# Kernel optimization log

Hardware: AMD Instinct MI355X
Metric: run time of the kernel (lower is better)

Reference implementation:

```python
import jax, jax.numpy as jnp
import numpy as np

CHUNK = 128
EPS = 1e-6


def setup_inputs() -> dict:
    key = jax.random.key(0)
    k1, k2, k3 = jax.random.split(key, 3)
    B, H, N, D, E = 4, 8, 4096, 64, 64
    q = jax.random.uniform(k1, (B, H, N, D), dtype=jnp.float32)
    k = jax.random.uniform(k2, (B, H, N, D), dtype=jnp.float32)
    v = jax.random.normal(k3, (B, H, N, E), dtype=jnp.float32)
    return {"q": q, "k": k, "v": v, "inferrring_states": 1}


def reference(q, k, v, inferrring_states):
    # infer_hidden_states path: chunked causal linear attention with carried state.
    B, H, N, D = q.shape
    E = v.shape[-1]
    nc = N // CHUNK
    # [nc, B, H, CHUNK, *] for scan over chunks
    qc = jnp.moveaxis(q.reshape(B, H, nc, CHUNK, D), 2, 0)
    kc = jnp.moveaxis(k.reshape(B, H, nc, CHUNK, D), 2, 0)
    vc = jnp.moveaxis(v.reshape(B, H, nc, CHUNK, E), 2, 0)

    Z0 = jnp.zeros((B, H, 1, D), dtype=q.dtype)        # running sum of k
    S0 = jnp.zeros((B, H, 1, D, E), dtype=q.dtype)     # running sum of k v^T

    def step(carry, qkv):
        Z, S = carry
        qi, ki, vi = qkv
        k_cumsum = Z + jnp.cumsum(ki, axis=-2)                      # [B,H,C,D]
        D_inv = 1.0 / jnp.einsum('bhnd,bhnd->bhn', qi, k_cumsum + EPS)
        context = jnp.einsum('bhnd,bhne->bhnde', ki, vi)            # [B,H,C,D,E]
        ctx_cumsum = S + jnp.cumsum(context, axis=-3)
        out = jnp.einsum('bhnde,bhnd,bhn->bhne', ctx_cumsum, qi, D_inv)
        new_carry = (k_cumsum[:, :, -1:], ctx_cumsum[:, :, -1:])
        return new_carry, out

    (Z, S), outs = jax.lax.scan(step, (Z0, S0), (qc, kc, vc))
    out = jnp.moveaxis(outs, 0, 2).reshape(B, H, N, E)
    # states: Z=[B,H,D], S=[B,H,D,E]
    return out, Z[:, :, 0], S[:, :, 0]
```

## Files before the change

### kernel.cpp

```cpp
#include <hip/hip_runtime.h>


#define CHUNKSZ 128
#define DD 64
#define EE 64
#define NC 32
#define NBH 32
#define NSEQ 4096
#define EPSV 1e-6f
#define OUT0 (NBH * NSEQ * EE)
#define KV_ELEMS (NBH * NC * DD * EE)

typedef short bf16x8 __attribute__((ext_vector_type(8)));
typedef short bf16x4 __attribute__((ext_vector_type(4)));
typedef float f32x4  __attribute__((ext_vector_type(4)));

__device__ __forceinline__ unsigned short f2bf(float f) {
    union { float f; unsigned u; } x; x.f = f;
    unsigned u = x.u + 0x7FFFu + ((x.u >> 16) & 1u);
    return (unsigned short)(u >> 16);
}
__device__ __forceinline__ float bf2f(unsigned short s) {
    union { unsigned u; float f; } x; x.u = ((unsigned)s) << 16;
    return x.f;
}

__global__ __launch_bounds__(256) void la_phase1(
    const float* __restrict__ k, const float* __restrict__ v,
    float* __restrict__ kv, float* __restrict__ ks)
{
    const int blk = blockIdx.x;
    const int bh = blk / NC, c = blk % NC;
    const size_t rowbase = (size_t)bh * NSEQ + (size_t)c * CHUNKSZ;

    __shared__ alignas(16) unsigned short kT[CHUNKSZ * DD];
    __shared__ alignas(16) unsigned short vT[CHUNKSZ * EE];
    __shared__ float ksp[4][DD];

    char* kb = (char*)kT;
    char* vb = (char*)vT;

    const int t = threadIdx.x;
    const int w = t >> 6, l = t & 63;
    const int lg = l >> 4, lm = l & 15;

    float kpart[4] = {0.f, 0.f, 0.f, 0.f};
    {
        const float4* kg = (const float4*)(k + rowbase * DD);
        const float4* vg = (const float4*)(v + rowbase * EE);
        const int d0 = (t & 15) * 4;
#pragma unroll
        for (int i = 0; i < 8; ++i) {
            int idx = t + 256 * i;
            int m = idx >> 4;
            float4 f = kg[idx];
            kpart[0] += f.x; kpart[1] += f.y; kpart[2] += f.z; kpart[3] += f.w;
            int base = (m >> 3) * 1024 + (m & 7) * 2;
            *(unsigned short*)(kb + base + (d0 + 0) * 16) = f2bf(f.x);
            *(unsigned short*)(kb + base + (d0 + 1) * 16) = f2bf(f.y);
            *(unsigned short*)(kb + base + (d0 + 2) * 16) = f2bf(f.z);
            *(unsigned short*)(kb + base + (d0 + 3) * 16) = f2bf(f.w);
        }
#pragma unroll
        for (int i = 0; i < 8; ++i) {
            int idx = t + 256 * i;
            int m = idx >> 4;
            float4 f = vg[idx];
            int base = (m >> 3) * 1024 + (m & 7) * 2;
            *(unsigned short*)(vb + base + (d0 + 0) * 16) = f2bf(f.x);
            *(unsigned short*)(vb + base + (d0 + 1) * 16) = f2bf(f.y);
            *(unsigned short*)(vb + base + (d0 + 2) * 16) = f2bf(f.z);
            *(unsigned short*)(vb + base + (d0 + 3) * 16) = f2bf(f.w);
        }
    }
#pragma unroll
    for (int j = 0; j < 4; ++j) {
        kpart[j] += __shfl_xor(kpart[j], 16);
        kpart[j] += __shfl_xor(kpart[j], 32);
    }
    if (l < 16) {
#pragma unroll
        for (int j = 0; j < 4; ++j) ksp[w][l * 4 + j] = kpart[j];
    }
    __syncthreads();

    f32x4 acc[4] = {};
#pragma unroll
    for (int kk = 0; kk < 4; ++kk) {
        bf16x8 aK = *(bf16x8*)(kb + (lg + 4 * kk) * 1024 + (16 * w + lm) * 16);
#pragma unroll
        for (int ei = 0; ei < 4; ++ei) {
            bf16x8 bV = *(bf16x8*)(vb + (lg + 4 * kk) * 1024 + (16 * ei + lm) * 16);
            acc[ei] = __builtin_amdgcn_mfma_f32_16x16x32_bf16(aK, bV, acc[ei], 0, 0, 0);
        }
    }
    float* kvout = kv + (size_t)(bh * NC + c) * DD * EE;
#pragma unroll
    for (int ei = 0; ei < 4; ++ei) {
#pragma unroll
        for (int r = 0; r < 4; ++r) {
            int d = 16 * w + 4 * lg + r;
            kvout[(size_t)d * EE + 16 * ei + lm] = acc[ei][r];
        }
    }
    if (t < DD)
        ks[(size_t)(bh * NC + c) * DD + t] = ksp[0][t] + ksp[1][t] + ksp[2][t] + ksp[3][t];
}

__global__ __launch_bounds__(64) void la_phase2(
    float* __restrict__ kv, float* __restrict__ ks, float* __restrict__ out)
{
    const int bid = blockIdx.x, t = threadIdx.x;
    if (bid < 512) {
        const int gid = bid * 64 + t;
        const int bh = gid >> 10;
        const int rem = gid & 1023;
        float* base = kv + (size_t)bh * (NC * DD * EE) + (size_t)rem * 4;
        float4 vals[32];
#pragma unroll
        for (int c = 0; c < 32; ++c)
            vals[c] = *(const float4*)(base + (size_t)c * (DD * EE));
        float4 run = {0.f, 0.f, 0.f, 0.f};
#pragma unroll
        for (int c = 0; c < 32; ++c) {
            float4 x = vals[c];
            *(float4*)(base + (size_t)c * (DD * EE)) = run;
            run.x += x.x; run.y += x.y; run.z += x.z; run.w += x.w;
        }
        *(float4*)(out + OUT0 + NBH * DD + (size_t)gid * 4) = run;
    } else {
        const int tid = (bid - 512) * 64 + t;
        const int bh = tid >> 6, d = tid & 63;
        float vals[32];
#pragma unroll
        for (int c = 0; c < 32; ++c)
            vals[c] = ks[(size_t)(bh * NC + c) * DD + d];
        float run = 0.f;
#pragma unroll
        for (int c = 0; c < 32; ++c) {
            float x = vals[c];
            ks[(size_t)(bh * NC + c) * DD + d] = run;
            run += x;
        }
        out[OUT0 + tid] = run;
    }
}

__global__ __launch_bounds__(256) void la_phase3(
    const float* __restrict__ q, const float* __restrict__ k,
    const float* __restrict__ v, const float* __restrict__ kv,
    const float* __restrict__ ks, float* __restrict__ out)
{
    const int blk = blockIdx.x;
    const int bh = blk / NC, c = blk % NC;
    const size_t rowbase = (size_t)bh * NSEQ + (size_t)c * CHUNKSZ;

    __shared__ alignas(16) unsigned short k_lds[CHUNKSZ * DD];
    __shared__ alignas(16) unsigned short v_lds[CHUNKSZ * EE];
    __shared__ alignas(16) unsigned short s_lds[CHUNKSZ * CHUNKSZ];
    __shared__ alignas(16) unsigned short st_lds[DD * EE];
    __shared__ float dinv_lds[CHUNKSZ];

    char* kb  = (char*)k_lds;
    char* vb  = (char*)v_lds;
    char* sb  = (char*)s_lds;
    char* stb = (char*)st_lds;

    const int t  = threadIdx.x;
    const int w  = t >> 6;
    const int l  = t & 63;
    const int lg = l >> 4;
    const int lm = l & 15;

    {
        bf16x8 z = {0,0,0,0,0,0,0,0};
#pragma unroll
        for (int i = 0; i < 8; ++i)
            *(bf16x8*)(sb + t * 128 + i * 16) = z;
    }
    {
        const float4* kg = (const float4*)(k + rowbase * DD);
#pragma unroll
        for (int i = 0; i < 8; ++i) {
            int idx = t + i * 256;
            int m = idx >> 4, c4 = idx & 15;
            float4 f = kg[idx];
            bf16x4 u;
            u[0] = (short)f2bf(f.x); u[1] = (short)f2bf(f.y);
            u[2] = (short)f2bf(f.z); u[3] = (short)f2bf(f.w);
            int byt = m * 128 + ((c4 * 8) ^ ((m & 7) << 4));
            *(bf16x4*)(kb + byt) = u;
        }
    }
    {
        const float4* vg = (const float4*)(v + rowbase * EE);
#pragma unroll
        for (int i = 0; i < 8; ++i) {
            int idx = t + i * 256;
            int m = idx >> 4, e0 = (idx & 15) * 4;
            float4 f = vg[idx];
            int base = (m >> 3) * 1024 + (m & 7) * 2;
            *(unsigned short*)(vb + base + (e0 + 0) * 16) = f2bf(f.x);
            *(unsigned short*)(vb + base + (e0 + 1) * 16) = f2bf(f.y);
            *(unsigned short*)(vb + base + (e0 + 2) * 16) = f2bf(f.z);
            *(unsigned short*)(vb + base + (e0 + 3) * 16) = f2bf(f.w);
        }
    }
    {
        const float4* sg = (const float4*)(kv + ((size_t)(bh * NC + c) * DD) * EE);
#pragma unroll
        for (int i = 0; i < 4; ++i) {
            int idx = t + i * 256;
            int d = idx >> 4, e0 = (idx & 15) * 4;
            float4 f = sg[idx];
            float ff[4] = {f.x, f.y, f.z, f.w};
#pragma unroll
            for (int j = 0; j < 4; ++j) {
                int e = e0 + j;
                int byt = e * 128 + ((d * 2) ^ ((e & 7) << 4));
                *(unsigned short*)(stb + byt) = f2bf(ff[j]);
            }
        }
    }
    bf16x8 a_q[2][2];
#pragma unroll
    for (int ni2 = 0; ni2 < 2; ++ni2) {
        int ni = w + 4 * ni2;
        const float* qrow = q + (rowbase + 16 * ni + lm) * DD;
#pragma unroll
        for (int kk = 0; kk < 2; ++kk) {
            const float4* p = (const float4*)(qrow + 8 * lg + 32 * kk);
            float4 f0 = p[0], f1 = p[1];
            bf16x8 u;
            u[0] = (short)f2bf(f0.x); u[1] = (short)f2bf(f0.y);
            u[2] = (short)f2bf(f0.z); u[3] = (short)f2bf(f0.w);
            u[4] = (short)f2bf(f1.x); u[5] = (short)f2bf(f1.y);
            u[6] = (short)f2bf(f1.z); u[7] = (short)f2bf(f1.w);
            a_q[ni2][kk] = u;
        }
    }
    __syncthreads();

#pragma unroll
    for (int ni2 = 0; ni2 < 2; ++ni2) {
        const int ni = w + 4 * ni2;
        for (int mi = 0; mi <= ni; ++mi) {
            f32x4 cc = {0.f, 0.f, 0.f, 0.f};
            const int m = 16 * mi + lm;
#pragma unroll
            for (int kk = 0; kk < 2; ++kk) {
                int byt = m * 128 + (((8 * lg + 32 * kk) * 2) ^ ((m & 7) << 4));
                bf16x8 bk = *(bf16x8*)(kb + byt);
                cc = __builtin_amdgcn_mfma_f32_16x16x32_bf16(a_q[ni2][kk], bk, cc, 0, 0, 0);
            }
            const int nbase = 16 * ni + 4 * lg;
#pragma unroll
            for (int r = 0; r < 4; ++r) {
                int n = nbase + r;
                float val = (m <= n) ? cc[r] : 0.f;
                int byt = n * 256 + ((m * 2) ^ ((n & 7) << 4));
                *(unsigned short*)(sb + byt) = f2bf(val);
            }
        }
    }
    __syncthreads();

    {
        const int n = t >> 1, h = t & 1;
        float ssum = 0.f;
#pragma unroll
        for (int s8 = 0; s8 < 8; ++s8) {
            int byt = n * 256 + ((128 * h + 16 * s8) ^ ((n & 7) << 4));
            bf16x8 sv = *(bf16x8*)(sb + byt);
#pragma unroll
            for (int j = 0; j < 8; ++j) ssum += bf2f((unsigned short)sv[j]);
        }
        const float* qrow = q + (rowbase + n) * DD + 32 * h;
        const float* Zi = ks + (size_t)(bh * NC + c) * DD + 32 * h;
        float qdot = 0.f, qs = 0.f;
#pragma unroll
        for (int d = 0; d < 32; ++d) {
            float qf = qrow[d];
            qdot += qf * Zi[d];
            qs += qf;
        }
        float tot = ssum + qdot + EPSV * qs;
        tot += __shfl_xor(tot, 1);
        if (h == 0) dinv_lds[n] = 1.f / tot;
    }

    f32x4 acc[2][4];
#pragma unroll
    for (int ni2 = 0; ni2 < 2; ++ni2) {
        const int ni = w + 4 * ni2;
        const int kmax = (ni >> 1) + 1;
#pragma unroll
        for (int ei = 0; ei < 4; ++ei) {
            f32x4 cc = {0.f, 0.f, 0.f, 0.f};
            const int e = 16 * ei + lm;
#pragma unroll
            for (int kk = 0; kk < 2; ++kk) {
                int byt = e * 128 + (((8 * lg + 32 * kk) * 2) ^ ((e & 7) << 4));
                bf16x8 bs = *(bf16x8*)(stb + byt);
                cc = __builtin_amdgcn_mfma_f32_16x16x32_bf16(a_q[ni2][kk], bs, cc, 0, 0, 0);
            }
            const int n = 16 * ni + lm;
            for (int kk = 0; kk < kmax; ++kk) {
                int bytA = n * 256 + (((8 * lg + 32 * kk) * 2) ^ ((n & 7) << 4));
                bf16x8 as = *(bf16x8*)(sb + bytA);
                int bytB = (lg + 4 * kk) * 1024 + e * 16;
                bf16x8 bv = *(bf16x8*)(vb + bytB);
                cc = __builtin_amdgcn_mfma_f32_16x16x32_bf16(as, bv, cc, 0, 0, 0);
            }
            acc[ni2][ei] = cc;
        }
    }
    __syncthreads();

#pragma unroll
    for (int ni2 = 0; ni2 < 2; ++ni2) {
        const int nbase = 16 * (w + 4 * ni2) + 4 * lg;
#pragma unroll
        for (int ei = 0; ei < 4; ++ei) {
            const int e = 16 * ei + lm;
#pragma unroll
            for (int r = 0; r < 4; ++r) {
                int n = nbase + r;
                out[(rowbase + n) * EE + e] = acc[ni2][ei][r] * dinv_lds[n];
            }
        }
    }
}

extern "C" void kernel_launch(void* const* d_in, const int* in_sizes, int n_in,
                              void* d_out, int out_size, void* d_ws, size_t ws_size,
                              hipStream_t stream)
{
    (void)in_sizes; (void)n_in; (void)out_size; (void)ws_size;
    const float* q = (const float*)d_in[0];
    const float* k = (const float*)d_in[1];
    const float* v = (const float*)d_in[2];
    float* out = (float*)d_out;
    float* kv = (float*)d_ws;
    float* ks = kv + KV_ELEMS;

    la_phase1<<<NBH * NC, 256, 0, stream>>>(k, v, kv, ks);
    la_phase2<<<544, 64, 0, stream>>>(kv, ks, out);
    la_phase3<<<NBH * NC, 256, 0, stream>>>(q, k, v, kv, ks, out);
}
```

Before: 58.52 us.

## Store per-chunk KV states as transposed bf16 to halve workspace traffic

Phase 1 now writes each chunk's K^T V partial state as bf16 in an E-major (transposed) layout instead of fp32. Phase 2 prefix-sums these with fp32 accumulators but stores the exclusive prefixes back as bf16, using half as many blocks. Phase 3 then loads them with 16-byte vector copies straight into its swizzled LDS tile, with no per-element conversion or scatter. This cuts workspace read/write bytes across all three kernels, but it rounds the intermediate prefix states to bf16 before they reach phase 3.

```diff
diff --git a/kernel.cpp b/kernel.cpp
--- a/kernel.cpp
+++ b/kernel.cpp
@@ -27,7 +27,7 @@
 
 __global__ __launch_bounds__(256) void la_phase1(
     const float* __restrict__ k, const float* __restrict__ v,
-    float* __restrict__ kv, float* __restrict__ ks)
+    unsigned short* __restrict__ kvT, float* __restrict__ ks)
 {
     const int blk = blockIdx.x;
     const int bh = blk / NC, c = blk % NC;
@@ -94,50 +94,56 @@
             acc[ei] = __builtin_amdgcn_mfma_f32_16x16x32_bf16(aK, bV, acc[ei], 0, 0, 0);
         }
     }
-    float* kvout = kv + (size_t)(bh * NC + c) * DD * EE;
+    unsigned short* kvout = kvT + (size_t)(bh * NC + c) * DD * EE;
 #pragma unroll
     for (int ei = 0; ei < 4; ++ei) {
-#pragma unroll
-        for (int r = 0; r < 4; ++r) {
-            int d = 16 * w + 4 * lg + r;
-            kvout[(size_t)d * EE + 16 * ei + lm] = acc[ei][r];
-        }
+        bf16x4 u;
+        u[0] = (short)f2bf(acc[ei][0]); u[1] = (short)f2bf(acc[ei][1]);
+        u[2] = (short)f2bf(acc[ei][2]); u[3] = (short)f2bf(acc[ei][3]);
+        *(bf16x4*)(kvout + (16 * ei + lm) * DD + 16 * w + 4 * lg) = u;
     }
     if (t < DD)
         ks[(size_t)(bh * NC + c) * DD + t] = ksp[0][t] + ksp[1][t] + ksp[2][t] + ksp[3][t];
 }
 
 __global__ __launch_bounds__(64) void la_phase2(
-    float* __restrict__ kv, float* __restrict__ ks, float* __restrict__ out)
+    unsigned short* __restrict__ kvT, float* __restrict__ ks, float* __restrict__ out)
 {
     const int bid = blockIdx.x, t = threadIdx.x;
-    if (bid < 512) {
+    if (bid < 256) {
         const int gid = bid * 64 + t;
-        const int bh = gid >> 10;
-        const int rem = gid & 1023;
-        float* base = kv + (size_t)bh * (NC * DD * EE) + (size_t)rem * 4;
-        float4 vals[32];
-#pragma unroll
-        for (int c = 0; c < 32; ++c)
-            vals[c] = *(const float4*)(base + (size_t)c * (DD * EE));
-        float4 run = {0.f, 0.f, 0.f, 0.f};
-#pragma unroll
-        for (int c = 0; c < 32; ++c) {
-            float4 x = vals[c];
-            *(float4*)(base + (size_t)c * (DD * EE)) = run;
-            run.x += x.x; run.y += x.y; run.z += x.z; run.w += x.w;
-        }
-        *(float4*)(out + OUT0 + NBH * DD + (size_t)gid * 4) = run;
+        const int bh = gid >> 9;
+        const int g = gid & 511;
+        unsigned short* base = kvT + (size_t)bh * (NC * DD * EE) + (size_t)g * 8;
+        bf16x8 vals[NC];
+#pragma unroll
+        for (int c = 0; c < NC; ++c)
+            vals[c] = *(const bf16x8*)(base + (size_t)c * (DD * EE));
+        float run[8] = {};
+#pragma unroll
+        for (int c = 0; c < NC; ++c) {
+            bf16x8 pr;
+#pragma unroll
+            for (int j = 0; j < 8; ++j) pr[j] = (short)f2bf(run[j]);
+            *(bf16x8*)(base + (size_t)c * (DD * EE)) = pr;
+#pragma unroll
+            for (int j = 0; j < 8; ++j) run[j] += bf2f((unsigned short)vals[c][j]);
+        }
+        const int e = g >> 3, d0 = (g & 7) * 8;
+        float* Sout = out + OUT0 + NBH * DD + (size_t)bh * DD * EE;
+#pragma unroll
+        for (int j = 0; j < 8; ++j)
+            Sout[(size_t)(d0 + j) * EE + e] = run[j];
     } else {
-        const int tid = (bid - 512) * 64 + t;
+        const int tid = (bid - 256) * 64 + t;
         const int bh = tid >> 6, d = tid & 63;
-        float vals[32];
-#pragma unroll
-        for (int c = 0; c < 32; ++c)
+        float vals[NC];
+#pragma unroll
+        for (int c = 0; c < NC; ++c)
             vals[c] = ks[(size_t)(bh * NC + c) * DD + d];
         float run = 0.f;
 #pragma unroll
-        for (int c = 0; c < 32; ++c) {
+        for (int c = 0; c < NC; ++c) {
             float x = vals[c];
             ks[(size_t)(bh * NC + c) * DD + d] = run;
             run += x;
@@ -148,7 +154,7 @@
 
 __global__ __launch_bounds__(256) void la_phase3(
     const float* __restrict__ q, const float* __restrict__ k,
-    const float* __restrict__ v, const float* __restrict__ kv,
+    const float* __restrict__ v, const unsigned short* __restrict__ kvT,
     const float* __restrict__ ks, float* __restrict__ out)
 {
     const int blk = blockIdx.x;
@@ -207,19 +213,14 @@
         }
     }
     {
-        const float4* sg = (const float4*)(kv + ((size_t)(bh * NC + c) * DD) * EE);
-#pragma unroll
-        for (int i = 0; i < 4; ++i) {
-            int idx = t + i * 256;
-            int d = idx >> 4, e0 = (idx & 15) * 4;
-            float4 f = sg[idx];
-            float ff[4] = {f.x, f.y, f.z, f.w};
-#pragma unroll
-            for (int j = 0; j < 4; ++j) {
-                int e = e0 + j;
-                int byt = e * 128 + ((d * 2) ^ ((e & 7) << 4));
-                *(unsigned short*)(stb + byt) = f2bf(ff[j]);
-            }
+        const unsigned short* sg = kvT + (size_t)(bh * NC + c) * DD * EE;
+#pragma unroll
+        for (int i = 0; i < 2; ++i) {
+            int idx = t + 256 * i;
+            int e = idx >> 3;
+            bf16x8 x = *(const bf16x8*)(sg + (size_t)idx * 8);
+            int byt = e * 128 + (((idx & 7) * 16) ^ ((e & 7) << 4));
+            *(bf16x8*)(stb + byt) = x;
         }
     }
     bf16x8 a_q[2][2];
@@ -341,10 +342,10 @@
     const float* k = (const float*)d_in[1];
     const float* v = (const float*)d_in[2];
     float* out = (float*)d_out;
-    float* kv = (float*)d_ws;
-    float* ks = kv + KV_ELEMS;
-
-    la_phase1<<<NBH * NC, 256, 0, stream>>>(k, v, kv, ks);
-    la_phase2<<<544, 64, 0, stream>>>(kv, ks, out);
-    la_phase3<<<NBH * NC, 256, 0, stream>>>(q, k, v, kv, ks, out);
-}
+    unsigned short* kvT = (unsigned short*)d_ws;
+    float* ks = (float*)(kvT + KV_ELEMS);
+
+    la_phase1<<<NBH * NC, 256, 0, stream>>>(k, v, kvT, ks);
+    la_phase2<<<288, 64, 0, stream>>>(kvT, ks, out);
+    la_phase3<<<NBH * NC, 256, 0, stream>>>(q, k, v, kvT, ks, out);
+}
```

Measured after the change: 54.98 us. 1.06x faster.
